# Kernel optimization log

Measured on AMD Instinct MI355X. Metric: run time of the kernel, lower is better.

Reference implementation:

```python
import jax, jax.numpy as jnp
import numpy as np

N_NODES = 50000
N_EDGES = 800000
DIM = 100

def setup_inputs() -> dict:
    key = jax.random.key(0)
    k1, k2, k3, k4, k5, k6 = jax.random.split(key, 6)
    ego_embedding = jax.random.normal(k1, (N_NODES, DIM), dtype=jnp.float32)
    edge_src = jax.random.randint(k2, (N_EDGES,), 0, N_NODES, dtype=jnp.int32)
    edge_dst = jax.random.randint(k3, (N_EDGES,), 0, N_NODES, dtype=jnp.int32)
    edge_weight = jax.random.uniform(k4, (N_EDGES,), dtype=jnp.float32)
    W = jax.random.normal(k5, (DIM, DIM), dtype=jnp.float32) * (1.0 / np.sqrt(DIM))
    b = jax.random.normal(k6, (DIM,), dtype=jnp.float32) * 0.01
    return {"ego_embedding": ego_embedding, "edge_src": edge_src,
            "edge_dst": edge_dst, "edge_weight": edge_weight, "W": W, "b": b}

def reference(ego_embedding, edge_src, edge_dst, edge_weight, W, b):
    # Linear projection: h = x @ W^T + b  (torch Linear convention)
    hidden = ego_embedding @ W.T + b                    # [N, D]
    # u_mul_e: message on each edge = h[src] * edge_weight
    msgs = hidden[edge_src] * edge_weight[:, None]       # [E, D]
    # sum reduce into destination nodes
    out = jax.ops.segment_sum(msgs, edge_dst, num_segments=N_NODES)  # [N, D]
    return out
```

## Files before the change

### kernel.cpp

```cpp
#include <hip/hip_runtime.h>

#define N_NODES 50000
#define N_EDGES 800000
#define DIM 100

#define NB      1563
#define CAPB    768
#define OVF_CAP 4096
#define EPB     4096
#define BIN_BLOCKS  196
#define GEMM_BLOCKS 625
#define ROWS_PB 80

#define HIDB_OFF  0u
#define GCUR_OFF  10000000u
#define OVFC_OFF  10006256u
#define OVF_OFF   10006272u
#define BKT2_OFF  10071808u
#define WTU_OFF   19674880u
#define WS_NEED   19694880u

__device__ inline unsigned bf16hi(float v) {
    unsigned u = __float_as_uint(v);
    u += 0x7FFFu + ((u >> 16) & 1u);
    return u & 0xFFFF0000u;
}
__device__ inline unsigned bf16pair(float lo, float hi) {
    unsigned ulo = __float_as_uint(lo); ulo += 0x7FFFu + ((ulo >> 16) & 1u);
    unsigned uhi = __float_as_uint(hi); uhi += 0x7FFFu + ((uhi >> 16) & 1u);
    return (ulo >> 16) | (uhi & 0xFFFF0000u);
}
#define BFLO(u) __uint_as_float((u) << 16)
#define BFHI(u) __uint_as_float((u) & 0xFFFF0000u)

__global__ __launch_bounds__(256) void srgnn_transpose(
    const float* __restrict__ W, unsigned* __restrict__ WtU,
    int* __restrict__ gcur, int* __restrict__ ovfc)
{
    const unsigned i = blockIdx.x * 256u + threadIdx.x;
    if (i < DIM * 50) {
        const int k = i / 50, c2 = i - k * 50;
        WtU[i] = bf16pair(W[(2 * c2) * DIM + k], W[(2 * c2 + 1) * DIM + k]);
    }
    if (i < NB) gcur[i] = 0;
    if (i == 0) *ovfc = 0;
}

__global__ __launch_bounds__(256) void srgnn_gemm_bin(
    const float* __restrict__ x, const unsigned* __restrict__ WtU,
    const float* __restrict__ b, unsigned* __restrict__ hidU,
    const int* __restrict__ esrc, const int* __restrict__ edst,
    const float* __restrict__ ew, int* __restrict__ gcur,
    int* __restrict__ ovfc, int4* __restrict__ ovf, uint2* __restrict__ bkt2)
{
    __shared__ __align__(16) char smem[32000];
    const int t = threadIdx.x;

    if (blockIdx.x < BIN_BLOCKS) {
        int* hist = (int*)smem;
        int* lcur = hist + NB;
        const int e0 = blockIdx.x * EPB;

        for (int i = t; i < NB; i += 256) hist[i] = 0;
        __syncthreads();

        int d[16];
        #pragma unroll
        for (int k = 0; k < 16; ++k) {
            const int e = e0 + t + k * 256;
            d[k] = (e < N_EDGES) ? edst[e] : -1;
            if (d[k] >= 0) atomicAdd(&hist[d[k] >> 5], 1);
        }
        __syncthreads();
        for (int i = t; i < NB; i += 256)
            if (hist[i]) lcur[i] = atomicAdd(&gcur[i], hist[i]);
        __syncthreads();
        #pragma unroll
        for (int k = 0; k < 16; ++k) {
            if (d[k] >= 0) {
                const int e = e0 + t + k * 256;
                const int s = esrc[e];
                const float w = ew[e];
                const int bq = d[k] >> 5;
                const int pos = atomicAdd(&lcur[bq], 1);
                if (pos < CAPB) {
                    bkt2[(size_t)bq * CAPB + pos] =
                        make_uint2((unsigned)s | bf16hi(w), (unsigned)d[k]);
                } else {
                    const int op = atomicAdd(ovfc, 1);
                    if (op < OVF_CAP) ovf[op] = make_int4(d[k], s, __float_as_int(w), 0);
                }
            }
        }
    } else {
        float (*xs)[DIM] = (float (*)[DIM])smem;
        const int row0 = (blockIdx.x - BIN_BLOCKS) * ROWS_PB;

        for (int i = t; i < ROWS_PB * 25; i += 256) {
            const int r = i / 25, c4 = (i - r * 25) * 4;
            const float4 v = *reinterpret_cast<const float4*>(
                &x[(size_t)(row0 + r) * DIM + c4]);
            *reinterpret_cast<float4*>(&xs[r][c4]) = v;
        }
        __syncthreads();

        if (t < 250) {
            const int g    = t / 25;
            const int c    = t - g * 25;
            const int c4   = c * 4;
            const int c2ix = c * 2;

            const float4 bv = *reinterpret_cast<const float4*>(&b[c4]);
            float4 acc[8];
            #pragma unroll
            for (int j = 0; j < 8; ++j) acc[j] = bv;

            for (int kq = 0; kq < 25; ++kq) {
                const int k0 = 4 * kq;
                const uint2 wu0 = *reinterpret_cast<const uint2*>(&WtU[(k0 + 0) * 50 + c2ix]);
                const uint2 wu1 = *reinterpret_cast<const uint2*>(&WtU[(k0 + 1) * 50 + c2ix]);
                const uint2 wu2 = *reinterpret_cast<const uint2*>(&WtU[(k0 + 2) * 50 + c2ix]);
                const uint2 wu3 = *reinterpret_cast<const uint2*>(&WtU[(k0 + 3) * 50 + c2ix]);
                const float w00 = BFLO(wu0.x), w01 = BFHI(wu0.x), w02 = BFLO(wu0.y), w03 = BFHI(wu0.y);
                const float w10 = BFLO(wu1.x), w11 = BFHI(wu1.x), w12 = BFLO(wu1.y), w13 = BFHI(wu1.y);
                const float w20 = BFLO(wu2.x), w21 = BFHI(wu2.x), w22 = BFLO(wu2.y), w23 = BFHI(wu2.y);
                const float w30 = BFLO(wu3.x), w31 = BFHI(wu3.x), w32 = BFLO(wu3.y), w33 = BFHI(wu3.y);

                #pragma unroll
                for (int j = 0; j < 8; ++j) {
                    const float4 xv = *reinterpret_cast<const float4*>(
                        &xs[g + 10 * j][k0]);
                    acc[j].x += xv.x * w00; acc[j].y += xv.x * w01;
                    acc[j].z += xv.x * w02; acc[j].w += xv.x * w03;
                    acc[j].x += xv.y * w10; acc[j].y += xv.y * w11;
                    acc[j].z += xv.y * w12; acc[j].w += xv.y * w13;
                    acc[j].x += xv.z * w20; acc[j].y += xv.z * w21;
                    acc[j].z += xv.z * w22; acc[j].w += xv.z * w23;
                    acc[j].x += xv.w * w30; acc[j].y += xv.w * w31;
                    acc[j].z += xv.w * w32; acc[j].w += xv.w * w33;
                }
            }
            #pragma unroll
            for (int j = 0; j < 8; ++j) {
                const int row = row0 + g + 10 * j;
                uint2 p;
                p.x = bf16pair(acc[j].x, acc[j].y);
                p.y = bf16pair(acc[j].z, acc[j].w);
                *reinterpret_cast<uint2*>(&hidU[(size_t)row * 50 + c2ix]) = p;
            }
        }
    }
}

__global__ __launch_bounds__(256) void srgnn_agg_s32(
    const unsigned* __restrict__ hidU, const int* __restrict__ gcur,
    const uint2* __restrict__ bkt2, const int* __restrict__ ovfc,
    const int4* __restrict__ ovf, float* __restrict__ out)
{
    __shared__ uint2    recs[CAPB];
    __shared__ unsigned srt[CAPB];
    __shared__ int nh[32], sc[32], cur[32];

    const int t = threadIdx.x;
    const int bq = blockIdx.x;
    int cntb = gcur[bq];
    if (cntb > CAPB) cntb = CAPB;

    if (t < 32) nh[t] = 0;
    __syncthreads();
    for (int i = t; i < cntb; i += 256) {
        const uint2 r = bkt2[(size_t)bq * CAPB + i];
        recs[i] = r;
        atomicAdd(&nh[r.y & 31], 1);
    }
    __syncthreads();
    if (t < 32) sc[t] = nh[t];
    __syncthreads();
    for (int ofs = 1; ofs < 32; ofs <<= 1) {
        int a = 0;
        if (t < 32 && t >= ofs) a = sc[t - ofs];
        __syncthreads();
        if (t < 32) sc[t] += a;
        __syncthreads();
    }
    if (t < 32) cur[t] = sc[t] - nh[t];
    __syncthreads();
    for (int i = t; i < cntb; i += 256) {
        const uint2 r = recs[i];
        const int pos = atomicAdd(&cur[r.y & 31], 1);
        srt[pos] = r.x;
    }
    __syncthreads();

    int oc = *ovfc;
    if (oc > OVF_CAP) oc = OVF_CAP;
    const int lane = t & 63;
    const int wid  = t >> 6;
    const bool active = (lane < 50);

    for (int q = 0; q < 8; ++q) {
        const int n  = wid * 8 + q;
        const int s1 = sc[n];
        const int s0 = s1 - nh[n];
        float2 acc = make_float2(0.f, 0.f);

        int p = s0;
        for (; p + 8 <= s1; p += 8) {
            unsigned r[8], h[8];
            #pragma unroll
            for (int j = 0; j < 8; ++j) r[j] = srt[p + j];
            if (active) {
                #pragma unroll
                for (int j = 0; j < 8; ++j)
                    h[j] = hidU[(size_t)(r[j] & 0xFFFFu) * 50 + lane];
                #pragma unroll
                for (int j = 0; j < 8; ++j) {
                    const float wj = __uint_as_float(r[j] & 0xFFFF0000u);
                    acc.x += wj * __uint_as_float(h[j] << 16);
                    acc.y += wj * __uint_as_float(h[j] & 0xFFFF0000u);
                }
            }
        }
        for (; p < s1; ++p) {
            const unsigned r = srt[p];
            const float wi = __uint_as_float(r & 0xFFFF0000u);
            if (active) {
                const unsigned h = hidU[(size_t)(r & 0xFFFFu) * 50 + lane];
                acc.x += wi * __uint_as_float(h << 16);
                acc.y += wi * __uint_as_float(h & 0xFFFF0000u);
            }
        }

        const int ng = bq * 32 + n;
        if (oc > 0) {
            for (int i = 0; i < oc; ++i) {
                const int4 v = ovf[i];
                if (v.x == ng && active) {
                    const unsigned h = hidU[(size_t)v.y * 50 + lane];
                    const float wi = __int_as_float(v.z);
                    acc.x += wi * __uint_as_float(h << 16);
                    acc.y += wi * __uint_as_float(h & 0xFFFF0000u);
                }
            }
        }
        if (ng < N_NODES && active)
            *reinterpret_cast<float2*>(&out[(size_t)ng * DIM + 2 * lane]) = acc;
    }
}

__global__ __launch_bounds__(256) void srgnn_gemm_bias(
    const float* __restrict__ x, const float* __restrict__ W,
    const float* __restrict__ b, float* __restrict__ hidden)
{
    __shared__ float Wt[DIM][DIM + 4];
    __shared__ float bs[DIM];
    __shared__ float xs[8][DIM];
    const int t = threadIdx.x;
    for (int i = t; i < DIM * DIM; i += 256) {
        int c = i / DIM, k = i - c * DIM;
        Wt[k][c] = W[i];
    }
    if (t < DIM) bs[t] = b[t];
    const int row0 = blockIdx.x * 8;
    for (int i = t; i < 8 * DIM; i += 256) {
        int r = i / DIM, k = i - r * DIM;
        int row = row0 + r;
        xs[r][k] = (row < N_NODES) ? x[row * DIM + k] : 0.0f;
    }
    __syncthreads();
    if (t < 200) {
        const int r  = t / 25;
        const int c4 = (t - r * 25) * 4;
        float acc0 = bs[c4 + 0], acc1 = bs[c4 + 1], acc2 = bs[c4 + 2], acc3 = bs[c4 + 3];
        for (int k = 0; k < DIM; ++k) {
            const float xv = xs[r][k];
            const float4 wv = *reinterpret_cast<const float4*>(&Wt[k][c4]);
            acc0 += xv * wv.x; acc1 += xv * wv.y; acc2 += xv * wv.z; acc3 += xv * wv.w;
        }
        const int row = row0 + r;
        if (row < N_NODES)
            *reinterpret_cast<float4*>(&hidden[row * DIM + c4]) =
                make_float4(acc0, acc1, acc2, acc3);
    }
}

__global__ __launch_bounds__(256) void srgnn_scatter_atomic(
    const float* __restrict__ hidden, const int* __restrict__ esrc,
    const int* __restrict__ edst, const float* __restrict__ ew,
    float* __restrict__ out)
{
    const unsigned gid = blockIdx.x * 256u + threadIdx.x;
    const unsigned e = gid / 25u;
    const unsigned j = gid - e * 25u;
    if (e >= N_EDGES) return;
    const int   s  = esrc[e];
    const int   d  = edst[e];
    const float wt = ew[e];
    const float4 h = *reinterpret_cast<const float4*>(&hidden[(size_t)s * DIM + j * 4]);
    float* op = &out[(size_t)d * DIM + j * 4];
    atomicAdd(op + 0, h.x * wt);
    atomicAdd(op + 1, h.y * wt);
    atomicAdd(op + 2, h.z * wt);
    atomicAdd(op + 3, h.w * wt);
}

extern "C" void kernel_launch(void* const* d_in, const int* in_sizes, int n_in,
                              void* d_out, int out_size, void* d_ws, size_t ws_size,
                              hipStream_t stream) {
    const float* x    = (const float*)d_in[0];
    const int*   esrc = (const int*)  d_in[1];
    const int*   edst = (const int*)  d_in[2];
    const float* ew   = (const float*)d_in[3];
    const float* W    = (const float*)d_in[4];
    const float* b    = (const float*)d_in[5];
    float* out = (float*)d_out;

    char* ws = (char*)d_ws;

    if (ws_size >= WS_NEED) {
        unsigned* hidU = (unsigned*)(ws + HIDB_OFF);
        int*      gcur = (int*)     (ws + GCUR_OFF);
        int*      ovfc = (int*)     (ws + OVFC_OFF);
        int4*     ovf  = (int4*)    (ws + OVF_OFF);
        uint2*    bkt2 = (uint2*)   (ws + BKT2_OFF);
        unsigned* WtU  = (unsigned*)(ws + WTU_OFF);

        srgnn_transpose<<<(DIM * 50 + 255) / 256, 256, 0, stream>>>(
            W, WtU, gcur, ovfc);
        srgnn_gemm_bin<<<BIN_BLOCKS + GEMM_BLOCKS, 256, 0, stream>>>(
            x, WtU, b, hidU, esrc, edst, ew, gcur, ovfc, ovf, bkt2);
        srgnn_agg_s32<<<NB, 256, 0, stream>>>(hidU, gcur, bkt2, ovfc, ovf, out);
    } else {
        float* hidden = (float*)ws;
        hipMemsetAsync(d_out, 0, (size_t)out_size * sizeof(float), stream);
        const int gemm_blocks = (N_NODES + 7) / 8;
        srgnn_gemm_bias<<<gemm_blocks, 256, 0, stream>>>(x, W, b, hidden);
        const long long work = (long long)N_EDGES * 25;
        const int scat_blocks = (int)((work + 255) / 256);
        srgnn_scatter_atomic<<<scat_blocks, 256, 0, stream>>>(hidden, esrc, edst, ew, out);
    }
}
```

Baseline: 70.42 us.

## Compute projection GEMM with bf16 MFMA and replace transpose kernel with memset

Replaces the scalar FMA projection GEMM with a per-wavefront 16x16x32 bf16 MFMA tile that loads x and W directly from global memory and converts them to bf16 in registers. The separate transpose/init kernel goes away; the bucket counters are cleared with a memset instead. This aims to cut the GEMM's ALU time and one kernel launch. In exchange, W fragments are reloaded from global memory by every wave, and outputs are written as scattered 16-bit stores.

```diff
diff --git a/kernel.cpp b/kernel.cpp
--- a/kernel.cpp
+++ b/kernel.cpp
@@ -9,16 +9,19 @@
 #define OVF_CAP 4096
 #define EPB     4096
 #define BIN_BLOCKS  196
-#define GEMM_BLOCKS 625
-#define ROWS_PB 80
+#define GEMM_BLOCKS 782
+#define N_ROWTILES 3125
 
 #define HIDB_OFF  0u
 #define GCUR_OFF  10000000u
 #define OVFC_OFF  10006256u
 #define OVF_OFF   10006272u
 #define BKT2_OFF  10071808u
-#define WTU_OFF   19674880u
-#define WS_NEED   19694880u
+#define WS_NEED   19674880u
+
+typedef __attribute__((ext_vector_type(8))) short short8;
+typedef __attribute__((ext_vector_type(4))) float f32x4;
+union frag { unsigned u[4]; short8 s; };
 
 __device__ inline unsigned bf16hi(float v) {
     unsigned u = __float_as_uint(v);
@@ -30,30 +33,15 @@
     unsigned uhi = __float_as_uint(hi); uhi += 0x7FFFu + ((uhi >> 16) & 1u);
     return (ulo >> 16) | (uhi & 0xFFFF0000u);
 }
-#define BFLO(u) __uint_as_float((u) << 16)
-#define BFHI(u) __uint_as_float((u) & 0xFFFF0000u)
-
-__global__ __launch_bounds__(256) void srgnn_transpose(
-    const float* __restrict__ W, unsigned* __restrict__ WtU,
-    int* __restrict__ gcur, int* __restrict__ ovfc)
-{
-    const unsigned i = blockIdx.x * 256u + threadIdx.x;
-    if (i < DIM * 50) {
-        const int k = i / 50, c2 = i - k * 50;
-        WtU[i] = bf16pair(W[(2 * c2) * DIM + k], W[(2 * c2 + 1) * DIM + k]);
-    }
-    if (i < NB) gcur[i] = 0;
-    if (i == 0) *ovfc = 0;
-}
 
 __global__ __launch_bounds__(256) void srgnn_gemm_bin(
-    const float* __restrict__ x, const unsigned* __restrict__ WtU,
-    const float* __restrict__ b, unsigned* __restrict__ hidU,
+    const float* __restrict__ x, const float* __restrict__ W,
+    const float* __restrict__ b, unsigned short* __restrict__ hid16,
     const int* __restrict__ esrc, const int* __restrict__ edst,
     const float* __restrict__ ew, int* __restrict__ gcur,
     int* __restrict__ ovfc, int4* __restrict__ ovf, uint2* __restrict__ bkt2)
 {
-    __shared__ __align__(16) char smem[32000];
+    __shared__ __align__(16) char smem[12544];
     const int t = threadIdx.x;
 
     if (blockIdx.x < BIN_BLOCKS) {
@@ -93,60 +81,70 @@
             }
         }
     } else {
-        float (*xs)[DIM] = (float (*)[DIM])smem;
-        const int row0 = (blockIdx.x - BIN_BLOCKS) * ROWS_PB;
-
-        for (int i = t; i < ROWS_PB * 25; i += 256) {
-            const int r = i / 25, c4 = (i - r * 25) * 4;
-            const float4 v = *reinterpret_cast<const float4*>(
-                &x[(size_t)(row0 + r) * DIM + c4]);
-            *reinterpret_cast<float4*>(&xs[r][c4]) = v;
-        }
-        __syncthreads();
-
-        if (t < 250) {
-            const int g    = t / 25;
-            const int c    = t - g * 25;
-            const int c4   = c * 4;
-            const int c2ix = c * 2;
-
-            const float4 bv = *reinterpret_cast<const float4*>(&b[c4]);
-            float4 acc[8];
+        const int gb = blockIdx.x - BIN_BLOCKS;
+        const int wv = gb * 4 + (t >> 6);
+        if (wv >= N_ROWTILES) return;
+        const int l   = t & 63;
+        const int r16 = l & 15;
+        const int kg  = l >> 4;
+        const int row = wv * 16 + r16;
+
+        frag A[4];
+        #pragma unroll
+        for (int kt = 0; kt < 4; ++kt) {
+            float4 fa = make_float4(0.f, 0.f, 0.f, 0.f);
+            float4 fb = make_float4(0.f, 0.f, 0.f, 0.f);
+            if (kt < 3) {
+                const float* px = &x[(size_t)row * DIM + kt * 32 + kg * 8];
+                fa = *reinterpret_cast<const float4*>(px);
+                fb = *reinterpret_cast<const float4*>(px + 4);
+            } else if (kg == 0) {
+                fa = *reinterpret_cast<const float4*>(&x[(size_t)row * DIM + 96]);
+            }
+            A[kt].u[0] = bf16pair(fa.x, fa.y);
+            A[kt].u[1] = bf16pair(fa.z, fa.w);
+            A[kt].u[2] = bf16pair(fb.x, fb.y);
+            A[kt].u[3] = bf16pair(fb.z, fb.w);
+        }
+
+        for (int ct = 0; ct < 7; ++ct) {
+            const int col = ct * 16 + r16;
+            const bool cok = (col < DIM);
+            frag B[4];
             #pragma unroll
-            for (int j = 0; j < 8; ++j) acc[j] = bv;
-
-            for (int kq = 0; kq < 25; ++kq) {
-                const int k0 = 4 * kq;
-                const uint2 wu0 = *reinterpret_cast<const uint2*>(&WtU[(k0 + 0) * 50 + c2ix]);
-                const uint2 wu1 = *reinterpret_cast<const uint2*>(&WtU[(k0 + 1) * 50 + c2ix]);
-                const uint2 wu2 = *reinterpret_cast<const uint2*>(&WtU[(k0 + 2) * 50 + c2ix]);
-                const uint2 wu3 = *reinterpret_cast<const uint2*>(&WtU[(k0 + 3) * 50 + c2ix]);
-                const float w00 = BFLO(wu0.x), w01 = BFHI(wu0.x), w02 = BFLO(wu0.y), w03 = BFHI(wu0.y);
-                const float w10 = BFLO(wu1.x), w11 = BFHI(wu1.x), w12 = BFLO(wu1.y), w13 = BFHI(wu1.y);
-                const float w20 = BFLO(wu2.x), w21 = BFHI(wu2.x), w22 = BFLO(wu2.y), w23 = BFHI(wu2.y);
-                const float w30 = BFLO(wu3.x), w31 = BFHI(wu3.x), w32 = BFLO(wu3.y), w33 = BFHI(wu3.y);
-
+            for (int kt = 0; kt < 4; ++kt) {
+                float4 fa = make_float4(0.f, 0.f, 0.f, 0.f);
+                float4 fb = make_float4(0.f, 0.f, 0.f, 0.f);
+                if (cok) {
+                    if (kt < 3) {
+                        const float* pw = &W[(size_t)col * DIM + kt * 32 + kg * 8];
+                        fa = *reinterpret_cast<const float4*>(pw);
+                        fb = *reinterpret_cast<const float4*>(pw + 4);
+                    } else if (kg == 0) {
+                        fa = *reinterpret_cast<const float4*>(&W[(size_t)col * DIM + 96]);
+                    }
+                }
+                B[kt].u[0] = bf16pair(fa.x, fa.y);
+                B[kt].u[1] = bf16pair(fa.z, fa.w);
+                B[kt].u[2] = bf16pair(fb.x, fb.y);
+                B[kt].u[3] = bf16pair(fb.z, fb.w);
+            }
+            f32x4 acc = {0.f, 0.f, 0.f, 0.f};
+            #pragma unroll
+            for (int kt = 0; kt < 4; ++kt)
+                acc = __builtin_amdgcn_mfma_f32_16x16x32_bf16(
+                    A[kt].s, B[kt].s, acc, 0, 0, 0);
+
+            if (cok) {
+                const float bc = b[col];
                 #pragma unroll
-                for (int j = 0; j < 8; ++j) {
-                    const float4 xv = *reinterpret_cast<const float4*>(
-                        &xs[g + 10 * j][k0]);
-                    acc[j].x += xv.x * w00; acc[j].y += xv.x * w01;
-                    acc[j].z += xv.x * w02; acc[j].w += xv.x * w03;
-                    acc[j].x += xv.y * w10; acc[j].y += xv.y * w11;
-                    acc[j].z += xv.y * w12; acc[j].w += xv.y * w13;
-                    acc[j].x += xv.z * w20; acc[j].y += xv.z * w21;
-                    acc[j].z += xv.z * w22; acc[j].w += xv.z * w23;
-                    acc[j].x += xv.w * w30; acc[j].y += xv.w * w31;
-                    acc[j].z += xv.w * w32; acc[j].w += xv.w * w33;
-                }
-            }
-            #pragma unroll
-            for (int j = 0; j < 8; ++j) {
-                const int row = row0 + g + 10 * j;
-                uint2 p;
-                p.x = bf16pair(acc[j].x, acc[j].y);
-                p.y = bf16pair(acc[j].z, acc[j].w);
-                *reinterpret_cast<uint2*>(&hidU[(size_t)row * 50 + c2ix]) = p;
+                for (int reg = 0; reg < 4; ++reg) {
+                    const int orow = wv * 16 + kg * 4 + reg;
+                    float v = acc[reg] + bc;
+                    unsigned uu = __float_as_uint(v);
+                    uu += 0x7FFFu + ((uu >> 16) & 1u);
+                    hid16[(size_t)orow * DIM + col] = (unsigned short)(uu >> 16);
+                }
             }
         }
     }
@@ -318,17 +316,16 @@
     char* ws = (char*)d_ws;
 
     if (ws_size >= WS_NEED) {
+        unsigned short* hid16 = (unsigned short*)(ws + HIDB_OFF);
         unsigned* hidU = (unsigned*)(ws + HIDB_OFF);
         int*      gcur = (int*)     (ws + GCUR_OFF);
+        int4*     ovf  = (int4*)    (ws + OVF_OFF);
         int*      ovfc = (int*)     (ws + OVFC_OFF);
-        int4*     ovf  = (int4*)    (ws + OVF_OFF);
         uint2*    bkt2 = (uint2*)   (ws + BKT2_OFF);
-        unsigned* WtU  = (unsigned*)(ws + WTU_OFF);
-
-        srgnn_transpose<<<(DIM * 50 + 255) / 256, 256, 0, stream>>>(
-            W, WtU, gcur, ovfc);
+
+        hipMemsetAsync(gcur, 0, (OVFC_OFF - GCUR_OFF) + 16, stream);
         srgnn_gemm_bin<<<BIN_BLOCKS + GEMM_BLOCKS, 256, 0, stream>>>(
-            x, WtU, b, hidU, esrc, edst, ew, gcur, ovfc, ovf, bkt2);
+            x, W, b, hid16, esrc, edst, ew, gcur, ovfc, ovf, bkt2);
         srgnn_agg_s32<<<NB, 256, 0, stream>>>(hidU, gcur, bkt2, ovfc, ovf, out);
     } else {
         float* hidden = (float*)ws;
```

After: 67.94 us. 3.5% less time.
